# Optimization experiments

Hardware: AMD Instinct MI355X
Metric: run time of the kernel (lower is better)

Reference implementation:

```python
import jax, jax.numpy as jnp
import numpy as np

B, S, HID = 2, 2048, 3072
NH, NKV, HD = 16, 8, 256
N_REP = NH // NKV
BITS, BLK = 4, 128
THETA = 10000.0
NEG = -1e9


def quantize_bfp(x, bits=BITS, block_size=BLK):
    """Block-floating-point quantization: blocks of `block_size` along the last
    (head_dim) axis share one power-of-two exponent; mantissas get `bits` levels
    (sign + bits-1), round-to-nearest."""
    shape = x.shape
    xb = x.reshape(-1, block_size)
    maxabs = jnp.max(jnp.abs(xb), axis=-1, keepdims=True)
    e = jnp.floor(jnp.log2(jnp.maximum(maxabs, 1e-30)))
    scale = jnp.exp2(e - (bits - 2))  # largest mantissa ~ 2^(bits-1)-1 covers maxabs
    qmax = 2.0 ** (bits - 1) - 1.0
    q = jnp.clip(jnp.round(xb / scale), -qmax, qmax) * scale
    q = jnp.where(maxabs > 0, q, 0.0)
    return q.reshape(shape)


def rotate_half(x):
    x1, x2 = jnp.split(x, 2, axis=-1)
    return jnp.concatenate((-x2, x1), axis=-1)


def setup_inputs() -> dict:
    key = jax.random.key(0)
    ks = jax.random.split(key, 5)
    hidden_states = jax.random.normal(ks[0], (B, S, HID), dtype=jnp.float32)
    sd = 0.02
    Wq = jax.random.normal(ks[1], (NH * HD, HID), dtype=jnp.float32) * sd
    Wk = jax.random.normal(ks[2], (NKV * HD, HID), dtype=jnp.float32) * sd
    Wv = jax.random.normal(ks[3], (NKV * HD, HID), dtype=jnp.float32) * sd
    Wo = jax.random.normal(ks[4], (HID, NH * HD), dtype=jnp.float32) * sd
    # rotary tables (HF convention: concat(freqs, freqs))
    pos = jnp.arange(S, dtype=jnp.float32)
    inv_freq = 1.0 / (THETA ** (jnp.arange(0, HD, 2, dtype=jnp.float32) / HD))
    freqs = jnp.einsum('s,d->sd', pos, inv_freq)
    emb = jnp.concatenate((freqs, freqs), axis=-1)  # (S, HD)
    cos = jnp.cos(emb)[None]  # (1, S, HD)
    sin = jnp.sin(emb)[None]
    # additive causal mask (B, 1, S, S)
    causal = jnp.where(jnp.tril(jnp.ones((S, S), dtype=bool)), 0.0, NEG).astype(jnp.float32)
    attention_mask = jnp.broadcast_to(causal[None, None], (B, 1, S, S))
    return {"hidden_states": hidden_states, "Wq": Wq, "Wk": Wk, "Wv": Wv,
            "Wo": Wo, "cos": cos, "sin": sin, "attention_mask": attention_mask}


def reference(hidden_states, Wq, Wk, Wv, Wo, cos, sin, attention_mask):
    b, s, _ = hidden_states.shape
    q = jnp.einsum('bsh,dh->bsd', hidden_states, Wq).reshape(b, s, NH, HD).transpose(0, 2, 1, 3)
    k = jnp.einsum('bsh,dh->bsd', hidden_states, Wk).reshape(b, s, NKV, HD).transpose(0, 2, 1, 3)
    v = jnp.einsum('bsh,dh->bsd', hidden_states, Wv).reshape(b, s, NKV, HD).transpose(0, 2, 1, 3)
    # RoPE (cos/sin unsqueezed at dim 1 -> (1,1,S,HD))
    c, sn = cos[:, None], sin[:, None]
    q = q * c + rotate_half(q) * sn
    k = k * c + rotate_half(k) * sn
    # int4 BFP quantization of keys (along rows of head_dim)
    k = quantize_bfp(k)
    # GQA: repeat kv heads
    k = jnp.repeat(k, N_REP, axis=1)
    v = jnp.repeat(v, N_REP, axis=1)
    scores = jnp.einsum('bhqd,bhkd->bhqk', q, k) / jnp.sqrt(jnp.float32(HD))
    scores = scores + attention_mask
    attn = jax.nn.softmax(scores.astype(jnp.float32), axis=-1).astype(q.dtype)
    out = jnp.einsum('bhqk,bhkd->bhqd', attn, v)
    out = out.transpose(0, 2, 1, 3).reshape(b, s, NH * HD)
    return jnp.einsum('bsd,hd->bsh', out, Wo)
```

## Files before the change

### kernel.cpp

```cpp
#include <hip/hip_runtime.h>
#include <math.h>

#define Bsz 2
#define Ssz 2048
#define HIDs 3072
#define NHs 16
#define NKVs 8
#define HDs 256

typedef _Float16 f16;
typedef _Float16 f16x8 __attribute__((ext_vector_type(8)));
typedef _Float16 f16x4 __attribute__((ext_vector_type(4)));
typedef float f32x4 __attribute__((ext_vector_type(4)));

__device__ __forceinline__ void async16(const f16* g, f16* l) {
    __builtin_amdgcn_global_load_lds(
        (const __attribute__((address_space(1))) void*)g,
        (__attribute__((address_space(3))) void*)l, 16, 0, 0);
}

__device__ __forceinline__ float row_max16(float v) {
    int t;
    t = __builtin_amdgcn_mov_dpp(__float_as_int(v), 0x121, 0xf, 0xf, false);
    v = fmaxf(v, __int_as_float(t));
    t = __builtin_amdgcn_mov_dpp(__float_as_int(v), 0x122, 0xf, 0xf, false);
    v = fmaxf(v, __int_as_float(t));
    t = __builtin_amdgcn_mov_dpp(__float_as_int(v), 0x124, 0xf, 0xf, false);
    v = fmaxf(v, __int_as_float(t));
    t = __builtin_amdgcn_mov_dpp(__float_as_int(v), 0x128, 0xf, 0xf, false);
    v = fmaxf(v, __int_as_float(t));
    return v;
}
__device__ __forceinline__ float row_sum16(float v) {
    int t;
    t = __builtin_amdgcn_mov_dpp(__float_as_int(v), 0x121, 0xf, 0xf, false);
    v = v + __int_as_float(t);
    t = __builtin_amdgcn_mov_dpp(__float_as_int(v), 0x122, 0xf, 0xf, false);
    v = v + __int_as_float(t);
    t = __builtin_amdgcn_mov_dpp(__float_as_int(v), 0x124, 0xf, 0xf, false);
    v = v + __int_as_float(t);
    t = __builtin_amdgcn_mov_dpp(__float_as_int(v), 0x128, 0xf, 0xf, false);
    v = v + __int_as_float(t);
    return v;
}

#define N4_HS  3145728
#define N4_WQ  3145728
#define N4_WK  1572864
#define N4_WV  1572864
#define N4_WO  3145728
#define N4_TOT (N4_HS + N4_WQ + N4_WK + N4_WV + N4_WO)

__global__ void cast_all_kernel(const float4* __restrict__ hs, const float4* __restrict__ wq,
                                const float4* __restrict__ wk, const float4* __restrict__ wv,
                                const float4* __restrict__ wo,
                                f16x4* __restrict__ hs_h, f16x4* __restrict__ wq_h,
                                f16x4* __restrict__ wk_h, f16x4* __restrict__ wv_h,
                                f16x4* __restrict__ wo_h) {
    int i = blockIdx.x * blockDim.x + threadIdx.x;
    const float4* src; f16x4* dst; int off;
    if (i < N4_HS)                       { src = hs; dst = hs_h; off = i; }
    else if (i < N4_HS + N4_WQ)          { src = wq; dst = wq_h; off = i - N4_HS; }
    else if (i < N4_HS + N4_WQ + N4_WK)  { src = wk; dst = wk_h; off = i - (N4_HS + N4_WQ); }
    else if (i < N4_TOT - N4_WO)         { src = wv; dst = wv_h; off = i - (N4_HS + N4_WQ + N4_WK); }
    else                                 { src = wo; dst = wo_h; off = i - (N4_TOT - N4_WO); }
    float4 v = src[off];
    f16x4 r;
    r[0] = (f16)v.x; r[1] = (f16)v.y; r[2] = (f16)v.z; r[3] = (f16)v.w;
    dst[off] = r;
}

__global__ __launch_bounds__(256) void gemm_nt_f16(
    const f16* __restrict__ A, const f16* __restrict__ Bm, float* __restrict__ C,
    int M, int N, int K)
{
    __shared__ __align__(16) f16 As[128 * 32];
    __shared__ __align__(16) f16 Bs[128 * 32];
    const int tid  = threadIdx.x;
    const int wave = tid >> 6, lane = tid & 63;
    const int l15  = lane & 15, quad = lane >> 4;
    const int m0 = blockIdx.y * 128, n0 = blockIdx.x * 128;
    const int wm = (wave >> 1) * 64, wn = (wave & 1) * 64;
    const int srow = wave * 32 + (lane >> 2);
    const int scol = (lane & 3) * 8;

    f32x4 acc[4][4];
    const f32x4 fz = {0.f, 0.f, 0.f, 0.f};
#pragma unroll
    for (int i = 0; i < 4; i++)
#pragma unroll
        for (int j = 0; j < 4; j++) acc[i][j] = fz;

    const f16* Ag0 = A  + (size_t)(m0 + srow) * K + scol;
    const f16* Ag1 = A  + (size_t)(m0 + srow + 16) * K + scol;
    const f16* Bg0 = Bm + (size_t)(n0 + srow) * K + scol;
    const f16* Bg1 = Bm + (size_t)(n0 + srow + 16) * K + scol;
    f16* Al0 = As + (wave * 32) * 32;
    f16* Al1 = As + (wave * 32 + 16) * 32;
    f16* Bl0 = Bs + (wave * 32) * 32;
    f16* Bl1 = Bs + (wave * 32 + 16) * 32;

    for (int k0 = 0; k0 < K; k0 += 32) {
        __syncthreads();
        async16(Ag0 + k0, Al0);
        async16(Ag1 + k0, Al1);
        async16(Bg0 + k0, Bl0);
        async16(Bg1 + k0, Bl1);
        __syncthreads();
        f16x8 af[4], bfr[4];
#pragma unroll
        for (int i = 0; i < 4; i++)
            af[i] = *(const f16x8*)(As + (wm + i * 16 + l15) * 32 + quad * 8);
#pragma unroll
        for (int j = 0; j < 4; j++)
            bfr[j] = *(const f16x8*)(Bs + (wn + j * 16 + l15) * 32 + quad * 8);
#pragma unroll
        for (int i = 0; i < 4; i++)
#pragma unroll
            for (int j = 0; j < 4; j++)
                acc[i][j] = __builtin_amdgcn_mfma_f32_16x16x32_f16(af[i], bfr[j], acc[i][j], 0, 0, 0);
    }
#pragma unroll
    for (int i = 0; i < 4; i++) {
        const int r = m0 + wm + i * 16 + quad * 4;
#pragma unroll
        for (int j = 0; j < 4; j++) {
            const int c = n0 + wn + j * 16 + l15;
#pragma unroll
            for (int rr = 0; rr < 4; rr++)
                C[(size_t)(r + rr) * N + c] = acc[i][j][rr];
        }
    }
}

__global__ void rope_q_kernel(const float* __restrict__ qp, const float* __restrict__ cosb,
                              const float* __restrict__ sinb, f16* __restrict__ qo) {
    const int s = blockIdx.x, h = blockIdx.y, b = blockIdx.z;
    const int d = threadIdx.x;
    const float* row = qp + (size_t)(b * Ssz + s) * (NHs * HDs) + h * HDs;
    float x = row[d];
    float other = (d < 128) ? -row[d + 128] : row[d - 128];
    float val = (x * cosb[s * HDs + d] + other * sinb[s * HDs + d]) * 0.0625f;
    qo[((size_t)(b * NHs + h) * Ssz + s) * HDs + d] = (f16)val;
}

__global__ void rope_quant_k_kernel(const float* __restrict__ kp, const float* __restrict__ cosb,
                                    const float* __restrict__ sinb, f16* __restrict__ ko) {
    const int s = blockIdx.x, h = blockIdx.y, b = blockIdx.z;
    const int d = threadIdx.x;
    const float* row = kp + (size_t)(b * Ssz + s) * (NKVs * HDs) + h * HDs;
    float x = row[d];
    float other = (d < 128) ? -row[d + 128] : row[d - 128];
    float val = x * cosb[s * HDs + d] + other * sinb[s * HDs + d];
    __shared__ float red[256];
    red[d] = fabsf(val);
    __syncthreads();
    for (int off = 64; off >= 1; off >>= 1) {
        if ((d & 127) < off) red[d] = fmaxf(red[d], red[d + off]);
        __syncthreads();
    }
    float maxabs = red[d & 128];
    float out;
    if (maxabs > 0.f) {
        int ex;
        frexpf(maxabs, &ex);
        float scale = ldexpf(1.0f, ex - 3);
        float q = rintf(val / scale);
        q = fminf(7.f, fmaxf(-7.f, q));
        out = q * scale;
    } else out = 0.f;
    ko[((size_t)(b * NKVs + h) * Ssz + s) * HDs + d] = (f16)out;
}

__global__ __launch_bounds__(256) void transpose_v_kernel(
    const float* __restrict__ proj, f16* __restrict__ vt)
{
    const int s0 = blockIdx.x * 64, c0 = blockIdx.y * 64, b = blockIdx.z;
    const int tid = threadIdx.x;
    __shared__ f16 T[64 * 72];
    {
        const int r = tid >> 2, cc = (tid & 3) * 16;
        const float* src = proj + (size_t)(b * Ssz + s0 + r) * (NKVs * HDs) + c0 + cc;
        f16 tmp[16];
#pragma unroll
        for (int q4 = 0; q4 < 4; q4++) {
            float4 v = *(const float4*)(src + q4 * 4);
            tmp[q4 * 4 + 0] = (f16)v.x; tmp[q4 * 4 + 1] = (f16)v.y;
            tmp[q4 * 4 + 2] = (f16)v.z; tmp[q4 * 4 + 3] = (f16)v.w;
        }
        *(f16x8*)(T + r * 72 + cc)     = *(f16x8*)(tmp);
        *(f16x8*)(T + r * 72 + cc + 8) = *(f16x8*)(tmp + 8);
    }
    __syncthreads();
    {
        const int d = tid >> 2, sc = (tid & 3) * 16;
        f16 tmp[16];
#pragma unroll
        for (int j = 0; j < 16; j++) tmp[j] = T[(sc + j) * 72 + d];
        const int col = c0 + d;
        const int kh = col >> 8, dd = col & 255;
        f16* dst = vt + ((size_t)(b * NKVs + kh) * HDs + dd) * Ssz + s0 + sc;
        *(f16x8*)(dst)     = *(f16x8*)(tmp);
        *(f16x8*)(dst + 8) = *(f16x8*)(tmp + 8);
    }
}

__global__ __launch_bounds__(256, 2) void attn_kernel(
    const f16* __restrict__ Q,
    const f16* __restrict__ Kq,
    const f16* __restrict__ Vt,
    f16* __restrict__ O)
{
    const int qt = (gridDim.x - 1) - blockIdx.x;
    const int h = blockIdx.y, b = blockIdx.z;
    const int kh = h >> 1;
    const int tid = threadIdx.x;
    const int wave = tid >> 6, lane = tid & 63;
    const int l15 = lane & 15, quad = lane >> 4;
    const int wrow = qt * 128 + wave * 32;

    const f16* Qb  = Q  + ((size_t)(b * NHs  + h)  * Ssz) * HDs;
    const f16* Kg  = Kq + ((size_t)(b * NKVs + kh) * Ssz) * HDs;
    const f16* Vtg = Vt + ((size_t)(b * NKVs + kh) * HDs) * Ssz;

    __shared__ __align__(16) f16 Ks[32 * 256];
    __shared__ __align__(16) f16 Vs[256 * 32];
    __shared__ __align__(16) f16 Pl[4 * 32 * 40];
    f16* Pw = Pl + wave * 32 * 40;

    const int k_r  = lane >> 5;
    const int k_cs = (lane & 31) ^ (k_r << 2);
    const int v_r  = lane >> 2;
    const int v_cs = ((lane & 3) ^ (v_r & 3)) * 8;

    f16x8 qf0[8], qf1[8];
    {
        const f16* qrow0 = Qb + (size_t)(wrow + l15) * HDs + quad * 8;
        const f16* qrow1 = qrow0 + (size_t)16 * HDs;
#pragma unroll
        for (int ks = 0; ks < 8; ks++) {
            qf0[ks] = *(const f16x8*)(qrow0 + ks * 32);
            qf1[ks] = *(const f16x8*)(qrow1 + ks * 32);
        }
    }

    const f32x4 fz = {0.f, 0.f, 0.f, 0.f};
    f32x4 accO0[16], accO1[16];
#pragma unroll
    for (int jn = 0; jn < 16; jn++) { accO0[jn] = fz; accO1[jn] = fz; }
    float mrow0[4], mrow1[4], lp0[4], lp1[4];
#pragma unroll
    for (int r = 0; r < 4; r++) { mrow0[r] = -1e30f; mrow1[r] = -1e30f; lp0[r] = 0.f; lp1[r] = 0.f; }

    const int nk = 4 * qt + 4;
    const int wave_max_row = wrow + 31;

    for (int kt = 0; kt < nk; kt++) {
        const int kvb = kt * 32;
        __syncthreads();
#pragma unroll
        for (int t = 0; t < 4; t++) {
            const int r2 = wave * 8 + t * 2;
            async16(Kg + (size_t)(kvb + r2 + k_r) * 256 + k_cs * 8, Ks + r2 * 256);
        }
#pragma unroll
        for (int t = 0; t < 4; t++) {
            const int d0 = wave * 64 + t * 16;
            async16(Vtg + (size_t)(d0 + v_r) * Ssz + kvb + v_cs, Vs + d0 * 32);
        }
        __syncthreads();

        if (kvb <= wave_max_row) {
            f32x4 s00 = fz, s01 = fz, s10 = fz, s11 = fz;
            const int sw0 = (l15 & 1) << 2;
#pragma unroll
            for (int ks = 0; ks < 8; ks++) {
                const int cpos = ((ks * 4 + quad) ^ sw0) * 8;
                f16x8 kf0 = *(const f16x8*)(Ks + l15 * 256 + cpos);
                f16x8 kf1 = *(const f16x8*)(Ks + (16 + l15) * 256 + cpos);
                s00 = __builtin_amdgcn_mfma_f32_16x16x32_f16(qf0[ks], kf0, s00, 0, 0, 0);
                s01 = __builtin_amdgcn_mfma_f32_16x16x32_f16(qf0[ks], kf1, s01, 0, 0, 0);
                s10 = __builtin_amdgcn_mfma_f32_16x16x32_f16(qf1[ks], kf0, s10, 0, 0, 0);
                s11 = __builtin_amdgcn_mfma_f32_16x16x32_f16(qf1[ks], kf1, s11, 0, 0, 0);
            }
            float a0[4], a1[4];
            bool need = false;
            const bool diag = (kvb + 31 > wrow);
#pragma unroll
            for (int r = 0; r < 4; r++) {
                float x0 = s00[r], x1 = s01[r];
                const int row0 = wrow + quad * 4 + r;
                if (diag) {
                    if (kvb + l15 > row0)      x0 = -1e30f;
                    if (kvb + 16 + l15 > row0) x1 = -1e30f;
                }
                float rmax = row_max16(fmaxf(x0, x1));
                float mold = mrow0[r];
                float mnew = fmaxf(mold, rmax);
                a0[r] = __expf(mold - mnew);
                need = need || (mnew > mold);
                float p0 = __expf(x0 - mnew);
                float p1 = __expf(x1 - mnew);
                lp0[r] = lp0[r] * a0[r] + (p0 + p1);
                mrow0[r] = mnew;
                Pw[(quad * 4 + r) * 40 + l15]      = (f16)p0;
                Pw[(quad * 4 + r) * 40 + 16 + l15] = (f16)p1;
                float y0 = s10[r], y1 = s11[r];
                const int row1 = row0 + 16;
                if (diag) {
                    if (kvb + l15 > row1)      y0 = -1e30f;
                    if (kvb + 16 + l15 > row1) y1 = -1e30f;
                }
                float rmax1 = row_max16(fmaxf(y0, y1));
                float mold1 = mrow1[r];
                float mnew1 = fmaxf(mold1, rmax1);
                a1[r] = __expf(mold1 - mnew1);
                need = need || (mnew1 > mold1);
                float q0 = __expf(y0 - mnew1);
                float q1 = __expf(y1 - mnew1);
                lp1[r] = lp1[r] * a1[r] + (q0 + q1);
                mrow1[r] = mnew1;
                Pw[(16 + quad * 4 + r) * 40 + l15]      = (f16)q0;
                Pw[(16 + quad * 4 + r) * 40 + 16 + l15] = (f16)q1;
            }
            if (__any(need)) {
#pragma unroll
                for (int jn = 0; jn < 16; jn++) {
                    f32x4 t0 = accO0[jn], t1 = accO1[jn];
                    t0[0] *= a0[0]; t0[1] *= a0[1]; t0[2] *= a0[2]; t0[3] *= a0[3];
                    t1[0] *= a1[0]; t1[1] *= a1[1]; t1[2] *= a1[2]; t1[3] *= a1[3];
                    accO0[jn] = t0; accO1[jn] = t1;
                }
            }
            f16x8 pf0 = *(const f16x8*)(Pw + l15 * 40 + quad * 8);
            f16x8 pf1 = *(const f16x8*)(Pw + (16 + l15) * 40 + quad * 8);
#pragma unroll
            for (int jn = 0; jn < 16; jn++) {
                f16x8 vf = *(const f16x8*)(Vs + (jn * 16 + l15) * 32 + ((quad ^ (l15 & 3))) * 8);
                accO0[jn] = __builtin_amdgcn_mfma_f32_16x16x32_f16(pf0, vf, accO0[jn], 0, 0, 0);
                accO1[jn] = __builtin_amdgcn_mfma_f32_16x16x32_f16(pf1, vf, accO1[jn], 0, 0, 0);
            }
        }
    }
#pragma unroll
    for (int r = 0; r < 4; r++) {
        const int row0 = wrow + quad * 4 + r;
        const float inv0 = 1.0f / row_sum16(lp0[r]);
        f16* orow0 = O + ((size_t)(b * Ssz) + row0) * (NHs * HDs) + h * HDs;
#pragma unroll
        for (int jn = 0; jn < 16; jn++)
            orow0[jn * 16 + l15] = (f16)(accO0[jn][r] * inv0);
        const int row1 = row0 + 16;
        const float inv1 = 1.0f / row_sum16(lp1[r]);
        f16* orow1 = O + ((size_t)(b * Ssz) + row1) * (NHs * HDs) + h * HDs;
#pragma unroll
        for (int jn = 0; jn < 16; jn++)
            orow1[jn * 16 + l15] = (f16)(accO1[jn][r] * inv1);
    }
}

extern "C" void kernel_launch(void* const* d_in, const int* in_sizes, int n_in,
                              void* d_out, int out_size, void* d_ws, size_t ws_size,
                              hipStream_t stream) {
    const float* hs   = (const float*)d_in[0];
    const float* Wq   = (const float*)d_in[1];
    const float* Wk   = (const float*)d_in[2];
    const float* Wv   = (const float*)d_in[3];
    const float* Wo   = (const float*)d_in[4];
    const float* cosb = (const float*)d_in[5];
    const float* sinb = (const float*)d_in[6];
    float* out = (float*)d_out;

    char* ws = (char*)d_ws;
    f16*   hs_h = (f16*)(ws);
    f16*   wo_h = (f16*)(ws + 25165824);
    float* proj = (float*)(ws + 50331648);
    f16*   q_h  = (f16*)(ws + 117440512);
    f16*   k_h  = (f16*)(ws + 150994944);
    f16*   vt_h = (f16*)(ws + 167772160);
    f16*   ao_h = (f16*)proj;

    cast_all_kernel<<<N4_TOT / 256, 256, 0, stream>>>(
        (const float4*)hs, (const float4*)Wq, (const float4*)Wk,
        (const float4*)Wv, (const float4*)Wo,
        (f16x4*)hs_h, (f16x4*)q_h, (f16x4*)k_h, (f16x4*)vt_h, (f16x4*)wo_h);

    gemm_nt_f16<<<dim3(4096 / 128, 4096 / 128), 256, 0, stream>>>(hs_h, q_h, proj, 4096, 4096, 3072);
    rope_q_kernel<<<dim3(Ssz, NHs, Bsz), 256, 0, stream>>>(proj, cosb, sinb, q_h);
    gemm_nt_f16<<<dim3(2048 / 128, 4096 / 128), 256, 0, stream>>>(hs_h, k_h, proj, 4096, 2048, 3072);
    rope_quant_k_kernel<<<dim3(Ssz, NKVs, Bsz), 256, 0, stream>>>(proj, cosb, sinb, k_h);
    gemm_nt_f16<<<dim3(2048 / 128, 4096 / 128), 256, 0, stream>>>(hs_h, vt_h, proj, 4096, 2048, 3072);
    transpose_v_kernel<<<dim3(Ssz / 64, (NKVs * HDs) / 64, Bsz), 256, 0, stream>>>(proj, vt_h);
    attn_kernel<<<dim3(Ssz / 128, NHs, Bsz), 256, 0, stream>>>(q_h, k_h, vt_h, ao_h);
    gemm_nt_f16<<<dim3(3072 / 128, 4096 / 128), 256, 0, stream>>>(ao_h, wo_h, out, 4096, 3072, 4096);
}
```

Before: 994.8 us.

## Double-buffer K/V LDS tiles, re-swizzle layouts, lazily rescale softmax max

K and V tiles now live in two LDS buffers, so the asynchronous global-to-LDS load of the next tile is issued before computing on the current one, with a single barrier at the end of each iteration instead of two. The XOR swizzle patterns for the K and V LDS layouts change, aiming to cut bank conflicts on the fragment reads. The online softmax now updates the running max only when a new row max exceeds the old one by more than 8, which skips most accumulator rescales and exp calls. The cost is doubled K/V LDS use (about 74KB per block), which may limit occupancy, and unnormalised probabilities up to about e^8 stored in fp16.

```diff
diff --git a/kernel.cpp b/kernel.cpp
--- a/kernel.cpp
+++ b/kernel.cpp
@@ -223,15 +223,30 @@
     const f16* Kg  = Kq + ((size_t)(b * NKVs + kh) * Ssz) * HDs;
     const f16* Vtg = Vt + ((size_t)(b * NKVs + kh) * HDs) * Ssz;
 
-    __shared__ __align__(16) f16 Ks[32 * 256];
-    __shared__ __align__(16) f16 Vs[256 * 32];
+    __shared__ __align__(16) f16 Ks[2][32 * 256];
+    __shared__ __align__(16) f16 Vs[2][256 * 32];
     __shared__ __align__(16) f16 Pl[4 * 32 * 40];
     f16* Pw = Pl + wave * 32 * 40;
 
     const int k_r  = lane >> 5;
-    const int k_cs = (lane & 31) ^ (k_r << 2);
+    const int k_c  = lane & 31;
     const int v_r  = lane >> 2;
-    const int v_cs = ((lane & 3) ^ (v_r & 3)) * 8;
+    const int v_gc = (lane & 3) ^ ((v_r >> 1) & 3);
+
+    auto stage = [&](int kt2, int bb) {
+        const int kvb_ = kt2 * 32;
+#pragma unroll
+        for (int t = 0; t < 4; t++) {
+            const int r2 = wave * 8 + t * 2;
+            const int gc = k_c ^ ((2 * t + k_r) & 7);
+            async16(Kg + (size_t)(kvb_ + r2 + k_r) * 256 + gc * 8, &Ks[bb][r2 * 256]);
+        }
+#pragma unroll
+        for (int t = 0; t < 4; t++) {
+            const int d0 = wave * 64 + t * 16;
+            async16(Vtg + (size_t)(d0 + v_r) * Ssz + kvb_ + v_gc * 8, &Vs[bb][d0 * 32]);
+        }
+    };
 
     f16x8 qf0[8], qf1[8];
     {
@@ -254,30 +269,26 @@
 
     const int nk = 4 * qt + 4;
     const int wave_max_row = wrow + 31;
+    const int kswz = l15 & 7;
+    const int vswz = (l15 >> 1) & 3;
+
+    stage(0, 0);
+    __syncthreads();
 
     for (int kt = 0; kt < nk; kt++) {
         const int kvb = kt * 32;
-        __syncthreads();
-#pragma unroll
-        for (int t = 0; t < 4; t++) {
-            const int r2 = wave * 8 + t * 2;
-            async16(Kg + (size_t)(kvb + r2 + k_r) * 256 + k_cs * 8, Ks + r2 * 256);
-        }
-#pragma unroll
-        for (int t = 0; t < 4; t++) {
-            const int d0 = wave * 64 + t * 16;
-            async16(Vtg + (size_t)(d0 + v_r) * Ssz + kvb + v_cs, Vs + d0 * 32);
-        }
-        __syncthreads();
+        const int cur = kt & 1;
+        if (kt + 1 < nk) stage(kt + 1, cur ^ 1);
+        const f16* Ksc = Ks[cur];
+        const f16* Vsc = Vs[cur];
 
         if (kvb <= wave_max_row) {
             f32x4 s00 = fz, s01 = fz, s10 = fz, s11 = fz;
-            const int sw0 = (l15 & 1) << 2;
 #pragma unroll
             for (int ks = 0; ks < 8; ks++) {
-                const int cpos = ((ks * 4 + quad) ^ sw0) * 8;
-                f16x8 kf0 = *(const f16x8*)(Ks + l15 * 256 + cpos);
-                f16x8 kf1 = *(const f16x8*)(Ks + (16 + l15) * 256 + cpos);
+                const int cpos = ((ks * 4 + quad) ^ kswz) * 8;
+                f16x8 kf0 = *(const f16x8*)(Ksc + l15 * 256 + cpos);
+                f16x8 kf1 = *(const f16x8*)(Ksc + (16 + l15) * 256 + cpos);
                 s00 = __builtin_amdgcn_mfma_f32_16x16x32_f16(qf0[ks], kf0, s00, 0, 0, 0);
                 s01 = __builtin_amdgcn_mfma_f32_16x16x32_f16(qf0[ks], kf1, s01, 0, 0, 0);
                 s10 = __builtin_amdgcn_mfma_f32_16x16x32_f16(qf1[ks], kf0, s10, 0, 0, 0);
@@ -296,9 +307,10 @@
                 }
                 float rmax = row_max16(fmaxf(x0, x1));
                 float mold = mrow0[r];
-                float mnew = fmaxf(mold, rmax);
-                a0[r] = __expf(mold - mnew);
-                need = need || (mnew > mold);
+                bool upd = rmax > mold + 8.f;
+                float mnew = upd ? rmax : mold;
+                a0[r] = upd ? __expf(mold - rmax) : 1.0f;
+                need = need || upd;
                 float p0 = __expf(x0 - mnew);
                 float p1 = __expf(x1 - mnew);
                 lp0[r] = lp0[r] * a0[r] + (p0 + p1);
@@ -313,9 +325,10 @@
                 }
                 float rmax1 = row_max16(fmaxf(y0, y1));
                 float mold1 = mrow1[r];
-                float mnew1 = fmaxf(mold1, rmax1);
-                a1[r] = __expf(mold1 - mnew1);
-                need = need || (mnew1 > mold1);
+                bool upd1 = rmax1 > mold1 + 8.f;
+                float mnew1 = upd1 ? rmax1 : mold1;
+                a1[r] = upd1 ? __expf(mold1 - rmax1) : 1.0f;
+                need = need || upd1;
                 float q0 = __expf(y0 - mnew1);
                 float q1 = __expf(y1 - mnew1);
                 lp1[r] = lp1[r] * a1[r] + (q0 + q1);
@@ -336,11 +349,12 @@
             f16x8 pf1 = *(const f16x8*)(Pw + (16 + l15) * 40 + quad * 8);
 #pragma unroll
             for (int jn = 0; jn < 16; jn++) {
-                f16x8 vf = *(const f16x8*)(Vs + (jn * 16 + l15) * 32 + ((quad ^ (l15 & 3))) * 8);
+                f16x8 vf = *(const f16x8*)(Vsc + (jn * 16 + l15) * 32 + (quad ^ vswz) * 8);
                 accO0[jn] = __builtin_amdgcn_mfma_f32_16x16x32_f16(pf0, vf, accO0[jn], 0, 0, 0);
                 accO1[jn] = __builtin_amdgcn_mfma_f32_16x16x32_f16(pf1, vf, accO1[jn], 0, 0, 0);
             }
         }
+        __syncthreads();
     }
 #pragma unroll
     for (int r = 0; r < 4; r++) {
```

After: 1.085 ms. 1.09x slower.
